# Kernel optimization log

Hardware: AMD Instinct MI355X
Metric: run time of the kernel (lower is better)

Reference implementation:

```python
import jax, jax.numpy as jnp
import numpy as np

N, E = 100000, 1600000
F_IN, F_HID, F_OUT = 64, 64, 16


def setup_inputs() -> dict:
    key = jax.random.key(0)
    ks = jax.random.split(key, 10)
    def g(k, shape):
        return jax.random.normal(k, shape, dtype=jnp.float32) * 0.05
    return {
        "x": jax.random.normal(ks[0], (N, F_IN), dtype=jnp.float32),
        "adj": jax.random.randint(ks[1], (2, E), 0, N, dtype=jnp.int32),
        # ChebConv K=2 params: per-order weights [in, out] + shared bias
        "W1_0": g(ks[2], (F_IN, F_HID)), "W1_1": g(ks[3], (F_IN, F_HID)),
        "b1": jnp.zeros((F_HID,), jnp.float32),
        "Wx_0": g(ks[4], (F_HID, F_HID)), "Wx_1": g(ks[5], (F_HID, F_HID)),
        "bx": jnp.zeros((F_HID,), jnp.float32),
        "W2_0": g(ks[6], (F_HID, F_OUT)), "W2_1": g(ks[7], (F_HID, F_OUT)),
        "b2": jnp.zeros((F_OUT,), jnp.float32),
    }


def _cheb(x, row, col, w, W0, W1, b):
    # K=2 Chebyshev conv: Tx0 = x, Tx1 = L_hat @ x (sparse propagate)
    n = x.shape[0]
    tx1 = jax.ops.segment_sum(w[:, None] * x[col], row, num_segments=n)
    return x @ W0 + tx1 @ W1 + b


def reference(x, adj, W1_0, W1_1, b1, Wx_0, Wx_1, bx, W2_0, W2_1, b2):
    row, col = adj[0], adj[1]
    n = x.shape[0]
    # sym-normalized Laplacian scaled by 2/lambda_max (=1): diagonal cancels,
    # off-diagonal weight = -deg^{-1/2}[row] * deg^{-1/2}[col]
    deg = jax.ops.segment_sum(jnp.ones(adj.shape[1], x.dtype), row, num_segments=n)
    dis = jnp.where(deg > 0, jax.lax.rsqrt(jnp.maximum(deg, 1e-12)), 0.0)
    w = -dis[row] * dis[col]
    h = jax.nn.relu(_cheb(x, row, col, w, W1_0, W1_1, b1))
    # dropout is identity in eval mode
    h = jax.nn.relu(_cheb(h, row, col, w, Wx_0, Wx_1, bx))
    return _cheb(h, row, col, w, W2_0, W2_1, b2)
```

## Files before the change

### kernel.cpp

```cpp
#include <hip/hip_runtime.h>
#include <hip/hip_bf16.h>


#define EPB 4096

typedef __attribute__((ext_vector_type(8))) short bf16x8;
typedef __attribute__((ext_vector_type(4))) float f32x4;

__device__ __forceinline__ float bf2f(unsigned short u) {
    unsigned int x = ((unsigned int)u) << 16;
    return __uint_as_float(x);
}
__device__ __forceinline__ unsigned short f2bf(float f) {
    unsigned int b = __float_as_uint(f);
    unsigned int r = (b + 0x7FFF + ((b >> 16) & 1)) >> 16;
    return (unsigned short)r;
}

__global__ __launch_bounds__(256) void zero_ints(int* __restrict__ p, int n) {
    int i = blockIdx.x * 256 + threadIdx.x;
    if (i < n) p[i] = 0;
}

template <int NC>
__device__ __forceinline__ void pack_pair(const float* __restrict__ W0,
                                          const float* __restrict__ W1,
                                          unsigned short* __restrict__ out, int idx) {
    constexpr int NT = NC / 16;
    int i = idx & 7;
    int m = (idx >> 3) & 15;
    int g = (idx >> 7) & 3;
    int f = idx >> 9;
    int nt = f % NT;
    int kt = f / NT;
    const float* W = (kt < 2) ? W0 : W1;
    int k = (kt & 1) * 32 + g * 8 + i;
    out[idx] = f2bf(W[k * NC + nt * 16 + m]);
}

__global__ __launch_bounds__(256) void wconv_all(const float* __restrict__ W1_0,
                                                 const float* __restrict__ W1_1,
                                                 const float* __restrict__ Wx_0,
                                                 const float* __restrict__ Wx_1,
                                                 const float* __restrict__ W2_0,
                                                 const float* __restrict__ W2_1,
                                                 unsigned short* __restrict__ wp1,
                                                 unsigned short* __restrict__ wpx,
                                                 unsigned short* __restrict__ wp2) {
    int idx = blockIdx.x * 256 + threadIdx.x;
    if (idx < 8192) pack_pair<64>(W1_0, W1_1, wp1, idx);
    else if (idx < 16384) pack_pair<64>(Wx_0, Wx_1, wpx, idx - 8192);
    else if (idx < 18432) pack_pair<16>(W2_0, W2_1, wp2, idx - 16384);
}

__global__ __launch_bounds__(256) void bucket_count(const int* __restrict__ row,
                                                    int* __restrict__ bcnt,
                                                    int e, int nbk) {
    __shared__ int bh[512];
    int tid = threadIdx.x;
    for (int j = tid; j < nbk; j += 256) bh[j] = 0;
    __syncthreads();
    int base = blockIdx.x * EPB;
#pragma unroll
    for (int k = 0; k < EPB / 256; ++k) {
        int i = base + k * 256 + tid;
        if (i < e) atomicAdd(&bh[row[i] >> 8], 1);
    }
    __syncthreads();
    for (int j = tid; j < nbk; j += 256) {
        int c = bh[j];
        if (c) atomicAdd(&bcnt[j], c);
    }
}

__global__ __launch_bounds__(256) void bucket_scan(const int* __restrict__ bcnt,
                                                   int* __restrict__ bbase,
                                                   int* __restrict__ bcursor,
                                                   int* __restrict__ off,
                                                   int nbk, int n, int e) {
    __shared__ int sa[512], sb[512];
    int tid = threadIdx.x;
    for (int j = tid; j < 512; j += 256) sa[j] = (j < nbk) ? bcnt[j] : 0;
    __syncthreads();
    int* in = sa;
    int* out = sb;
    for (int d = 1; d < 512; d <<= 1) {
        for (int j = tid; j < 512; j += 256)
            out[j] = in[j] + ((j >= d) ? in[j - d] : 0);
        __syncthreads();
        int* t = in; in = out; out = t;
    }
    for (int j = tid; j < nbk; j += 256) {
        int incl = in[j];
        int excl = incl - bcnt[j];
        bbase[j] = excl;
        bcursor[j] = excl;
        if (j == nbk - 1) bbase[nbk] = incl;
    }
    if (tid == 0) off[n] = e;
}

__global__ __launch_bounds__(256) void bucket_scatter(const int* __restrict__ row,
                                                      const int* __restrict__ col,
                                                      int* __restrict__ bcursor,
                                                      int* __restrict__ packed,
                                                      int e, int nbk) {
    __shared__ int bh[512];
    __shared__ int bbase[512];
    __shared__ int bcur[512];
    int tid = threadIdx.x;
    for (int j = tid; j < nbk; j += 256) { bh[j] = 0; bcur[j] = 0; }
    __syncthreads();
    int base = blockIdx.x * EPB;
#pragma unroll
    for (int k = 0; k < EPB / 256; ++k) {
        int i = base + k * 256 + tid;
        if (i < e) atomicAdd(&bh[row[i] >> 8], 1);
    }
    __syncthreads();
    for (int j = tid; j < nbk; j += 256) {
        int c = bh[j];
        bbase[j] = c ? atomicAdd(&bcursor[j], c) : 0;
    }
    __syncthreads();
#pragma unroll
    for (int k = 0; k < EPB / 256; ++k) {
        int i = base + k * 256 + tid;
        if (i < e) {
            int r = row[i];
            int b = r >> 8;
            int slot = bbase[b] + atomicAdd(&bcur[b], 1);
            packed[slot] = ((r & 255) << 17) | col[i];
        }
    }
}

__global__ __launch_bounds__(256) void bucket_build(const int* __restrict__ packed,
                                                    const int* __restrict__ bbase,
                                                    const float* __restrict__ x,
                                                    int* __restrict__ off,
                                                    float* __restrict__ dis,
                                                    int* __restrict__ csr,
                                                    unsigned short* __restrict__ y,
                                                    unsigned short* __restrict__ xb,
                                                    int n) {
    __shared__ int rcnt[256];
    __shared__ int sa[256], sb[256];
    __shared__ float disv[256];
    int tid = threadIdx.x;
    int b = blockIdx.x;
    int ebase = bbase[b], eend = bbase[b + 1];
    rcnt[tid] = 0;
    __syncthreads();
    for (int e = ebase + tid; e < eend; e += 256)
        atomicAdd(&rcnt[packed[e] >> 17], 1);
    __syncthreads();
    sa[tid] = rcnt[tid];
    __syncthreads();
    int* in = sa;
    int* out = sb;
    for (int d = 1; d < 256; d <<= 1) {
        out[tid] = in[tid] + ((tid >= d) ? in[tid - d] : 0);
        __syncthreads();
        int* t = in; in = out; out = t;
    }
    int grow = b * 256 + tid;
    int c = rcnt[tid];
    int excl = in[tid] - c;
    float dv = (c > 0) ? rsqrtf((float)c) : 0.0f;
    disv[tid] = dv;
    if (grow < n) {
        off[grow] = ebase + excl;
        dis[grow] = dv;
    }
    out[tid] = excl;
    __syncthreads();
    for (int e = ebase + tid; e < eend; e += 256) {
        int p = packed[e];
        int lr = p >> 17;
        int pos = atomicAdd(&out[lr], 1);
        csr[ebase + pos] = p & 0x1FFFF;
    }
    for (int idx = tid; idx < 4096; idx += 256) {
        int rr = idx >> 4, q = idx & 15;
        int R = b * 256 + rr;
        if (R < n) {
            float d = disv[rr];
            float4 v = ((const float4*)x)[(size_t)R * 16 + q];
            ushort4 o = {f2bf(v.x * d), f2bf(v.y * d), f2bf(v.z * d), f2bf(v.w * d)};
            ((ushort4*)y)[(size_t)R * 16 + q] = o;
            ushort4 xo = {f2bf(v.x), f2bf(v.y), f2bf(v.z), f2bf(v.w)};
            ((ushort4*)xb)[(size_t)R * 16 + q] = xo;
        }
    }
}


__global__ __launch_bounds__(256) void aggregate(const unsigned short* __restrict__ y,
                                                 const int* __restrict__ csr,
                                                 const int* __restrict__ off,
                                                 const float* __restrict__ dis,
                                                 unsigned short* __restrict__ tx, int n) {
    int tid = threadIdx.x;
    int r = blockIdx.x * 16 + (tid >> 4);
    if (r >= n) return;
    int q = tid & 15;
    int s0 = off[r], e1 = off[r + 1];
    const ushort4* Y = (const ushort4*)y;
    float ax = 0.f, ay = 0.f, az = 0.f, aw = 0.f;
    int t = s0;
    for (; t + 8 <= e1; t += 8) {
        int c0 = csr[t], c1 = csr[t + 1], c2 = csr[t + 2], c3 = csr[t + 3];
        int c4 = csr[t + 4], c5 = csr[t + 5], c6 = csr[t + 6], c7 = csr[t + 7];
        ushort4 v0 = Y[(size_t)c0 * 16 + q];
        ushort4 v1 = Y[(size_t)c1 * 16 + q];
        ushort4 v2 = Y[(size_t)c2 * 16 + q];
        ushort4 v3 = Y[(size_t)c3 * 16 + q];
        ushort4 v4 = Y[(size_t)c4 * 16 + q];
        ushort4 v5 = Y[(size_t)c5 * 16 + q];
        ushort4 v6 = Y[(size_t)c6 * 16 + q];
        ushort4 v7 = Y[(size_t)c7 * 16 + q];
        ax += ((bf2f(v0.x) + bf2f(v1.x)) + (bf2f(v2.x) + bf2f(v3.x))) +
              ((bf2f(v4.x) + bf2f(v5.x)) + (bf2f(v6.x) + bf2f(v7.x)));
        ay += ((bf2f(v0.y) + bf2f(v1.y)) + (bf2f(v2.y) + bf2f(v3.y))) +
              ((bf2f(v4.y) + bf2f(v5.y)) + (bf2f(v6.y) + bf2f(v7.y)));
        az += ((bf2f(v0.z) + bf2f(v1.z)) + (bf2f(v2.z) + bf2f(v3.z))) +
              ((bf2f(v4.z) + bf2f(v5.z)) + (bf2f(v6.z) + bf2f(v7.z)));
        aw += ((bf2f(v0.w) + bf2f(v1.w)) + (bf2f(v2.w) + bf2f(v3.w))) +
              ((bf2f(v4.w) + bf2f(v5.w)) + (bf2f(v6.w) + bf2f(v7.w)));
    }
    for (; t + 4 <= e1; t += 4) {
        int c0 = csr[t], c1 = csr[t + 1], c2 = csr[t + 2], c3 = csr[t + 3];
        ushort4 v0 = Y[(size_t)c0 * 16 + q];
        ushort4 v1 = Y[(size_t)c1 * 16 + q];
        ushort4 v2 = Y[(size_t)c2 * 16 + q];
        ushort4 v3 = Y[(size_t)c3 * 16 + q];
        ax += (bf2f(v0.x) + bf2f(v1.x)) + (bf2f(v2.x) + bf2f(v3.x));
        ay += (bf2f(v0.y) + bf2f(v1.y)) + (bf2f(v2.y) + bf2f(v3.y));
        az += (bf2f(v0.z) + bf2f(v1.z)) + (bf2f(v2.z) + bf2f(v3.z));
        aw += (bf2f(v0.w) + bf2f(v1.w)) + (bf2f(v2.w) + bf2f(v3.w));
    }
    for (; t < e1; ++t) {
        int c = csr[t];
        ushort4 v = Y[(size_t)c * 16 + q];
        ax += bf2f(v.x); ay += bf2f(v.y); az += bf2f(v.z); aw += bf2f(v.w);
    }
    float d = -dis[r];
    ushort4 o = {f2bf(ax * d), f2bf(ay * d), f2bf(az * d), f2bf(aw * d)};
    *(ushort4*)&tx[(size_t)r * 64 + q * 4] = o;
}


template <int NC, bool RELU, bool WRITE_HY>
__global__ __launch_bounds__(256) void dense_mfma(const unsigned short* __restrict__ A0,
                                                  const unsigned short* __restrict__ A1,
                                                  const unsigned short* __restrict__ Wp,
                                                  const float* __restrict__ bias,
                                                  const float* __restrict__ dis,
                                                  unsigned short* __restrict__ hout,
                                                  unsigned short* __restrict__ yout,
                                                  float* __restrict__ fout,
                                                  int n, int nrb) {
    constexpr int NT = NC / 16;
    int lane = threadIdx.x & 63;
    int m = lane & 15;
    int g = lane >> 4;
    const bf16x8* WP = (const bf16x8*)Wp;
    bf16x8 bf[NT][4];
#pragma unroll
    for (int kt = 0; kt < 4; ++kt)
#pragma unroll
        for (int nt = 0; nt < NT; ++nt)
            bf[nt][kt] = WP[((kt * NT + nt) * 4 + g) * 16 + m];
    int wrb = blockIdx.x * 4 + (threadIdx.x >> 6);
    int stride = gridDim.x * 4;
    for (int rb = wrb; rb < nrb; rb += stride) {
        int r0 = rb * 16;
        int ra = r0 + m;
        if (ra > n - 1) ra = n - 1;
        const unsigned short* q0 = A0 + (size_t)ra * 64 + g * 8;
        const unsigned short* q1 = A1 + (size_t)ra * 64 + g * 8;
        bf16x8 a0 = *(const bf16x8*)q0;
        bf16x8 a1 = *(const bf16x8*)(q0 + 32);
        bf16x8 a2 = *(const bf16x8*)q1;
        bf16x8 a3 = *(const bf16x8*)(q1 + 32);
        f32x4 acc[NT];
#pragma unroll
        for (int nt = 0; nt < NT; ++nt) {
            float b = bias[nt * 16 + m];
            acc[nt][0] = b; acc[nt][1] = b; acc[nt][2] = b; acc[nt][3] = b;
        }
#pragma unroll
        for (int nt = 0; nt < NT; ++nt) {
            acc[nt] = __builtin_amdgcn_mfma_f32_16x16x32_bf16(a0, bf[nt][0], acc[nt], 0, 0, 0);
            acc[nt] = __builtin_amdgcn_mfma_f32_16x16x32_bf16(a1, bf[nt][1], acc[nt], 0, 0, 0);
            acc[nt] = __builtin_amdgcn_mfma_f32_16x16x32_bf16(a2, bf[nt][2], acc[nt], 0, 0, 0);
            acc[nt] = __builtin_amdgcn_mfma_f32_16x16x32_bf16(a3, bf[nt][3], acc[nt], 0, 0, 0);
        }
#pragma unroll
        for (int reg = 0; reg < 4; ++reg) {
            int rr = r0 + 4 * g + reg;
            if (rr >= n) continue;
            if (WRITE_HY) {
                float dv = dis[rr];
#pragma unroll
                for (int nt = 0; nt < NT; ++nt) {
                    float v = acc[nt][reg];
                    if (RELU) v = fmaxf(v, 0.f);
                    hout[(size_t)rr * NC + nt * 16 + m] = f2bf(v);
                    yout[(size_t)rr * NC + nt * 16 + m] = f2bf(v * dv);
                }
            } else {
#pragma unroll
                for (int nt = 0; nt < NT; ++nt)
                    fout[(size_t)rr * NC + nt * 16 + m] = acc[nt][reg];
            }
        }
    }
}


extern "C" void kernel_launch(void* const* d_in, const int* in_sizes, int n_in,
                              void* d_out, int out_size, void* d_ws, size_t ws_size,
                              hipStream_t stream) {
    const float* x    = (const float*)d_in[0];
    const int*   adj  = (const int*)d_in[1];
    const float* W1_0 = (const float*)d_in[2];
    const float* W1_1 = (const float*)d_in[3];
    const float* b1   = (const float*)d_in[4];
    const float* Wx_0 = (const float*)d_in[5];
    const float* Wx_1 = (const float*)d_in[6];
    const float* bx   = (const float*)d_in[7];
    const float* W2_0 = (const float*)d_in[8];
    const float* W2_1 = (const float*)d_in[9];
    const float* b2   = (const float*)d_in[10];
    float* out = (float*)d_out;

    int N = in_sizes[0] / 64;
    int E = in_sizes[1] / 2;
    const int* row = adj;
    const int* col = adj + E;
    int NBK = (N + 255) / 256;
    int nRB = (N + 15) / 16;

    char* p = (char*)d_ws;
    auto alloc = [&](size_t bytes) {
        char* q = p;
        p += (bytes + 255) & ~(size_t)255;
        return q;
    };
    int*   bcnt  = (int*)alloc((size_t)(NBK) * 4);
    int*   bbase = (int*)alloc((size_t)(NBK + 1) * 4);
    int*   bcur  = (int*)alloc((size_t)(NBK) * 4);
    int*   off   = (int*)alloc((size_t)(N + 1) * 4);
    float* dis   = (float*)alloc((size_t)N * 4);
    int*   csr   = (int*)alloc((size_t)E * 4);
    unsigned short* wp1 = (unsigned short*)alloc(8192 * 2);
    unsigned short* wpx = (unsigned short*)alloc(8192 * 2);
    unsigned short* wp2 = (unsigned short*)alloc(2048 * 2);
    unsigned short* y  = (unsigned short*)alloc((size_t)N * 64 * 2);
    unsigned short* xb = (unsigned short*)alloc((size_t)N * 64 * 2);
    unsigned short* tx = (unsigned short*)alloc((size_t)N * 64 * 2);
    unsigned short* h  = (unsigned short*)alloc((size_t)N * 64 * 2);
    (void)ws_size;
    int* packed = (int*)tx;

    int EB = (E + EPB - 1) / EPB;
    zero_ints<<<(NBK + 255) / 256, 256, 0, stream>>>(bcnt, NBK);
    wconv_all<<<72, 256, 0, stream>>>(W1_0, W1_1, Wx_0, Wx_1, W2_0, W2_1, wp1, wpx, wp2);
    bucket_count<<<EB, 256, 0, stream>>>(row, bcnt, E, NBK);
    bucket_scan<<<1, 256, 0, stream>>>(bcnt, bbase, bcur, off, NBK, N, E);
    bucket_scatter<<<EB, 256, 0, stream>>>(row, col, bcur, packed, E, NBK);
    bucket_build<<<NBK, 256, 0, stream>>>(packed, bbase, x, off, dis, csr, y, xb, N);

    const int DG = 512;
    aggregate<<<(N + 15) / 16, 256, 0, stream>>>(y, csr, off, dis, tx, N);
    dense_mfma<64, true, true><<<DG, 256, 0, stream>>>(xb, tx, wp1, b1, dis, h, y, nullptr, N, nRB);
    aggregate<<<(N + 15) / 16, 256, 0, stream>>>(y, csr, off, dis, tx, N);
    dense_mfma<64, true, true><<<DG, 256, 0, stream>>>(h, tx, wpx, bx, dis, h, y, nullptr, N, nRB);
    aggregate<<<(N + 15) / 16, 256, 0, stream>>>(y, csr, off, dis, tx, N);
    dense_mfma<16, false, false><<<DG, 256, 0, stream>>>(h, tx, wp2, b2, dis, nullptr, nullptr, out, N, nRB);
}
```

Baseline: 202.7 us.

## Fuse sparse aggregation with dense MFMA per layer via LDS tile

Merges each layer's aggregate and dense_mfma kernels into one agg_dense kernel. The aggregated Tx1 tile is kept in swizzled shared memory instead of going through a global tx buffer. The gather now uses 4 threads per row with 16-byte bf16x8 loads, which needs double-buffered y/h arrays to avoid read-after-write hazards between layers. The zero_ints launch is folded into wconv_all. This removes three kernel launches and the tx write/read round trip, at the cost of less parallelism per row in the gather (4 lanes per row instead of 16) and extra workspace.

```diff
diff --git a/kernel.cpp b/kernel.cpp
--- a/kernel.cpp
+++ b/kernel.cpp
@@ -16,10 +16,9 @@
     unsigned int r = (b + 0x7FFF + ((b >> 16) & 1)) >> 16;
     return (unsigned short)r;
 }
-
-__global__ __launch_bounds__(256) void zero_ints(int* __restrict__ p, int n) {
-    int i = blockIdx.x * 256 + threadIdx.x;
-    if (i < n) p[i] = 0;
+__device__ __forceinline__ void acc8(float* a, bf16x8 v) {
+#pragma unroll
+    for (int i = 0; i < 8; ++i) a[i] += bf2f((unsigned short)(short)v[i]);
 }
 
 template <int NC>
@@ -46,8 +45,10 @@
                                                  const float* __restrict__ W2_1,
                                                  unsigned short* __restrict__ wp1,
                                                  unsigned short* __restrict__ wpx,
-                                                 unsigned short* __restrict__ wp2) {
+                                                 unsigned short* __restrict__ wp2,
+                                                 int* __restrict__ bcnt, int nbk) {
     int idx = blockIdx.x * 256 + threadIdx.x;
+    if (idx < nbk) bcnt[idx] = 0;
     if (idx < 8192) pack_pair<64>(W1_0, W1_1, wp1, idx);
     else if (idx < 16384) pack_pair<64>(Wx_0, Wx_1, wpx, idx - 8192);
     else if (idx < 18432) pack_pair<16>(W2_0, W2_1, wp2, idx - 16384);
@@ -196,75 +197,72 @@
 }
 
 
-__global__ __launch_bounds__(256) void aggregate(const unsigned short* __restrict__ y,
+template <int NC, bool RELU, bool WRITE_HY>
+__global__ __launch_bounds__(256) void agg_dense(const unsigned short* __restrict__ y,
+                                                 const unsigned short* __restrict__ A0,
                                                  const int* __restrict__ csr,
                                                  const int* __restrict__ off,
                                                  const float* __restrict__ dis,
-                                                 unsigned short* __restrict__ tx, int n) {
-    int tid = threadIdx.x;
-    int r = blockIdx.x * 16 + (tid >> 4);
-    if (r >= n) return;
-    int q = tid & 15;
-    int s0 = off[r], e1 = off[r + 1];
-    const ushort4* Y = (const ushort4*)y;
-    float ax = 0.f, ay = 0.f, az = 0.f, aw = 0.f;
-    int t = s0;
-    for (; t + 8 <= e1; t += 8) {
-        int c0 = csr[t], c1 = csr[t + 1], c2 = csr[t + 2], c3 = csr[t + 3];
-        int c4 = csr[t + 4], c5 = csr[t + 5], c6 = csr[t + 6], c7 = csr[t + 7];
-        ushort4 v0 = Y[(size_t)c0 * 16 + q];
-        ushort4 v1 = Y[(size_t)c1 * 16 + q];
-        ushort4 v2 = Y[(size_t)c2 * 16 + q];
-        ushort4 v3 = Y[(size_t)c3 * 16 + q];
-        ushort4 v4 = Y[(size_t)c4 * 16 + q];
-        ushort4 v5 = Y[(size_t)c5 * 16 + q];
-        ushort4 v6 = Y[(size_t)c6 * 16 + q];
-        ushort4 v7 = Y[(size_t)c7 * 16 + q];
-        ax += ((bf2f(v0.x) + bf2f(v1.x)) + (bf2f(v2.x) + bf2f(v3.x))) +
-              ((bf2f(v4.x) + bf2f(v5.x)) + (bf2f(v6.x) + bf2f(v7.x)));
-        ay += ((bf2f(v0.y) + bf2f(v1.y)) + (bf2f(v2.y) + bf2f(v3.y))) +
-              ((bf2f(v4.y) + bf2f(v5.y)) + (bf2f(v6.y) + bf2f(v7.y)));
-        az += ((bf2f(v0.z) + bf2f(v1.z)) + (bf2f(v2.z) + bf2f(v3.z))) +
-              ((bf2f(v4.z) + bf2f(v5.z)) + (bf2f(v6.z) + bf2f(v7.z)));
-        aw += ((bf2f(v0.w) + bf2f(v1.w)) + (bf2f(v2.w) + bf2f(v3.w))) +
-              ((bf2f(v4.w) + bf2f(v5.w)) + (bf2f(v6.w) + bf2f(v7.w)));
-    }
-    for (; t + 4 <= e1; t += 4) {
-        int c0 = csr[t], c1 = csr[t + 1], c2 = csr[t + 2], c3 = csr[t + 3];
-        ushort4 v0 = Y[(size_t)c0 * 16 + q];
-        ushort4 v1 = Y[(size_t)c1 * 16 + q];
-        ushort4 v2 = Y[(size_t)c2 * 16 + q];
-        ushort4 v3 = Y[(size_t)c3 * 16 + q];
-        ax += (bf2f(v0.x) + bf2f(v1.x)) + (bf2f(v2.x) + bf2f(v3.x));
-        ay += (bf2f(v0.y) + bf2f(v1.y)) + (bf2f(v2.y) + bf2f(v3.y));
-        az += (bf2f(v0.z) + bf2f(v1.z)) + (bf2f(v2.z) + bf2f(v3.z));
-        aw += (bf2f(v0.w) + bf2f(v1.w)) + (bf2f(v2.w) + bf2f(v3.w));
-    }
-    for (; t < e1; ++t) {
-        int c = csr[t];
-        ushort4 v = Y[(size_t)c * 16 + q];
-        ax += bf2f(v.x); ay += bf2f(v.y); az += bf2f(v.z); aw += bf2f(v.w);
-    }
-    float d = -dis[r];
-    ushort4 o = {f2bf(ax * d), f2bf(ay * d), f2bf(az * d), f2bf(aw * d)};
-    *(ushort4*)&tx[(size_t)r * 64 + q * 4] = o;
-}
-
-
-template <int NC, bool RELU, bool WRITE_HY>
-__global__ __launch_bounds__(256) void dense_mfma(const unsigned short* __restrict__ A0,
-                                                  const unsigned short* __restrict__ A1,
-                                                  const unsigned short* __restrict__ Wp,
-                                                  const float* __restrict__ bias,
-                                                  const float* __restrict__ dis,
-                                                  unsigned short* __restrict__ hout,
-                                                  unsigned short* __restrict__ yout,
-                                                  float* __restrict__ fout,
-                                                  int n, int nrb) {
+                                                 const unsigned short* __restrict__ Wp,
+                                                 const float* __restrict__ bias,
+                                                 unsigned short* __restrict__ hout,
+                                                 unsigned short* __restrict__ yout,
+                                                 float* __restrict__ fout,
+                                                 int n) {
     constexpr int NT = NC / 16;
-    int lane = threadIdx.x & 63;
+    __shared__ unsigned short txl[64 * 64];
+    int tid = threadIdx.x;
+
+    int row_l = tid >> 2;
+    int fq = tid & 3;
+    int r = blockIdx.x * 64 + row_l;
+    float acc16[16];
+#pragma unroll
+    for (int i = 0; i < 16; ++i) acc16[i] = 0.f;
+    float d = 0.f;
+    if (r < n) {
+        int s0 = off[r], e1 = off[r + 1];
+        const unsigned short* Yb = y + fq * 16;
+        int t = s0;
+        for (; t + 4 <= e1; t += 4) {
+            int c0 = csr[t], c1 = csr[t + 1], c2 = csr[t + 2], c3 = csr[t + 3];
+            const bf16x8* p0 = (const bf16x8*)(Yb + (size_t)c0 * 64);
+            const bf16x8* p1 = (const bf16x8*)(Yb + (size_t)c1 * 64);
+            const bf16x8* p2 = (const bf16x8*)(Yb + (size_t)c2 * 64);
+            const bf16x8* p3 = (const bf16x8*)(Yb + (size_t)c3 * 64);
+            bf16x8 v00 = p0[0], v01 = p0[1];
+            bf16x8 v10 = p1[0], v11 = p1[1];
+            bf16x8 v20 = p2[0], v21 = p2[1];
+            bf16x8 v30 = p3[0], v31 = p3[1];
+            acc8(acc16, v00); acc8(acc16 + 8, v01);
+            acc8(acc16, v10); acc8(acc16 + 8, v11);
+            acc8(acc16, v20); acc8(acc16 + 8, v21);
+            acc8(acc16, v30); acc8(acc16 + 8, v31);
+        }
+        for (; t < e1; ++t) {
+            int c = csr[t];
+            const bf16x8* pc = (const bf16x8*)(Yb + (size_t)c * 64);
+            bf16x8 v0 = pc[0], v1 = pc[1];
+            acc8(acc16, v0); acc8(acc16 + 8, v1);
+        }
+        d = -dis[r];
+    }
+    bf16x8 ov0, ov1;
+#pragma unroll
+    for (int i = 0; i < 8; ++i) {
+        ov0[i] = (short)f2bf(acc16[i] * d);
+        ov1[i] = (short)f2bf(acc16[8 + i] * d);
+    }
+    int swz = (row_l & 7) << 4;
+    int cb = fq * 32;
+    *(bf16x8*)((char*)txl + row_l * 128 + (cb ^ swz)) = ov0;
+    *(bf16x8*)((char*)txl + row_l * 128 + ((cb + 16) ^ swz)) = ov1;
+    __syncthreads();
+
+    int lane = tid & 63;
     int m = lane & 15;
     int g = lane >> 4;
+    int w = tid >> 6;
     const bf16x8* WP = (const bf16x8*)Wp;
     bf16x8 bf[NT][4];
 #pragma unroll
@@ -272,49 +270,46 @@
 #pragma unroll
         for (int nt = 0; nt < NT; ++nt)
             bf[nt][kt] = WP[((kt * NT + nt) * 4 + g) * 16 + m];
-    int wrb = blockIdx.x * 4 + (threadIdx.x >> 6);
-    int stride = gridDim.x * 4;
-    for (int rb = wrb; rb < nrb; rb += stride) {
-        int r0 = rb * 16;
-        int ra = r0 + m;
-        if (ra > n - 1) ra = n - 1;
-        const unsigned short* q0 = A0 + (size_t)ra * 64 + g * 8;
-        const unsigned short* q1 = A1 + (size_t)ra * 64 + g * 8;
-        bf16x8 a0 = *(const bf16x8*)q0;
-        bf16x8 a1 = *(const bf16x8*)(q0 + 32);
-        bf16x8 a2 = *(const bf16x8*)q1;
-        bf16x8 a3 = *(const bf16x8*)(q1 + 32);
-        f32x4 acc[NT];
-#pragma unroll
-        for (int nt = 0; nt < NT; ++nt) {
-            float b = bias[nt * 16 + m];
-            acc[nt][0] = b; acc[nt][1] = b; acc[nt][2] = b; acc[nt][3] = b;
-        }
-#pragma unroll
-        for (int nt = 0; nt < NT; ++nt) {
-            acc[nt] = __builtin_amdgcn_mfma_f32_16x16x32_bf16(a0, bf[nt][0], acc[nt], 0, 0, 0);
-            acc[nt] = __builtin_amdgcn_mfma_f32_16x16x32_bf16(a1, bf[nt][1], acc[nt], 0, 0, 0);
-            acc[nt] = __builtin_amdgcn_mfma_f32_16x16x32_bf16(a2, bf[nt][2], acc[nt], 0, 0, 0);
-            acc[nt] = __builtin_amdgcn_mfma_f32_16x16x32_bf16(a3, bf[nt][3], acc[nt], 0, 0, 0);
-        }
-#pragma unroll
-        for (int reg = 0; reg < 4; ++reg) {
-            int rr = r0 + 4 * g + reg;
-            if (rr >= n) continue;
-            if (WRITE_HY) {
-                float dv = dis[rr];
-#pragma unroll
-                for (int nt = 0; nt < NT; ++nt) {
-                    float v = acc[nt][reg];
-                    if (RELU) v = fmaxf(v, 0.f);
-                    hout[(size_t)rr * NC + nt * 16 + m] = f2bf(v);
-                    yout[(size_t)rr * NC + nt * 16 + m] = f2bf(v * dv);
-                }
-            } else {
-#pragma unroll
-                for (int nt = 0; nt < NT; ++nt)
-                    fout[(size_t)rr * NC + nt * 16 + m] = acc[nt][reg];
+    int r0 = blockIdx.x * 64 + w * 16;
+    int ra = r0 + m;
+    if (ra > n - 1) ra = n - 1;
+    const unsigned short* q0 = A0 + (size_t)ra * 64 + g * 8;
+    bf16x8 a0 = *(const bf16x8*)q0;
+    bf16x8 a1 = *(const bf16x8*)(q0 + 32);
+    int rl2 = w * 16 + m;
+    int sw2 = (m & 7) << 4;
+    bf16x8 a2 = *(bf16x8*)((char*)txl + rl2 * 128 + ((g * 16) ^ sw2));
+    bf16x8 a3 = *(bf16x8*)((char*)txl + rl2 * 128 + ((64 + g * 16) ^ sw2));
+    f32x4 acc[NT];
+#pragma unroll
+    for (int nt = 0; nt < NT; ++nt) {
+        float b = bias[nt * 16 + m];
+        acc[nt][0] = b; acc[nt][1] = b; acc[nt][2] = b; acc[nt][3] = b;
+    }
+#pragma unroll
+    for (int nt = 0; nt < NT; ++nt) {
+        acc[nt] = __builtin_amdgcn_mfma_f32_16x16x32_bf16(a0, bf[nt][0], acc[nt], 0, 0, 0);
+        acc[nt] = __builtin_amdgcn_mfma_f32_16x16x32_bf16(a1, bf[nt][1], acc[nt], 0, 0, 0);
+        acc[nt] = __builtin_amdgcn_mfma_f32_16x16x32_bf16(a2, bf[nt][2], acc[nt], 0, 0, 0);
+        acc[nt] = __builtin_amdgcn_mfma_f32_16x16x32_bf16(a3, bf[nt][3], acc[nt], 0, 0, 0);
+    }
+#pragma unroll
+    for (int reg = 0; reg < 4; ++reg) {
+        int rr = r0 + 4 * g + reg;
+        if (rr >= n) continue;
+        if (WRITE_HY) {
+            float dv = dis[rr];
+#pragma unroll
+            for (int nt = 0; nt < NT; ++nt) {
+                float v = acc[nt][reg];
+                if (RELU) v = fmaxf(v, 0.f);
+                hout[(size_t)rr * NC + nt * 16 + m] = f2bf(v);
+                yout[(size_t)rr * NC + nt * 16 + m] = f2bf(v * dv);
             }
+        } else {
+#pragma unroll
+            for (int nt = 0; nt < NT; ++nt)
+                fout[(size_t)rr * NC + nt * 16 + m] = acc[nt][reg];
         }
     }
 }
@@ -341,7 +336,6 @@
     const int* row = adj;
     const int* col = adj + E;
     int NBK = (N + 255) / 256;
-    int nRB = (N + 15) / 16;
 
     char* p = (char*)d_ws;
     auto alloc = [&](size_t bytes) {
@@ -355,29 +349,27 @@
     int*   off   = (int*)alloc((size_t)(N + 1) * 4);
     float* dis   = (float*)alloc((size_t)N * 4);
     int*   csr   = (int*)alloc((size_t)E * 4);
+    int*   packed = (int*)alloc((size_t)E * 4);
     unsigned short* wp1 = (unsigned short*)alloc(8192 * 2);
     unsigned short* wpx = (unsigned short*)alloc(8192 * 2);
     unsigned short* wp2 = (unsigned short*)alloc(2048 * 2);
     unsigned short* y  = (unsigned short*)alloc((size_t)N * 64 * 2);
+    unsigned short* y2 = (unsigned short*)alloc((size_t)N * 64 * 2);
     unsigned short* xb = (unsigned short*)alloc((size_t)N * 64 * 2);
-    unsigned short* tx = (unsigned short*)alloc((size_t)N * 64 * 2);
     unsigned short* h  = (unsigned short*)alloc((size_t)N * 64 * 2);
+    unsigned short* h2 = (unsigned short*)alloc((size_t)N * 64 * 2);
     (void)ws_size;
-    int* packed = (int*)tx;
 
     int EB = (E + EPB - 1) / EPB;
-    zero_ints<<<(NBK + 255) / 256, 256, 0, stream>>>(bcnt, NBK);
-    wconv_all<<<72, 256, 0, stream>>>(W1_0, W1_1, Wx_0, Wx_1, W2_0, W2_1, wp1, wpx, wp2);
+    wconv_all<<<72, 256, 0, stream>>>(W1_0, W1_1, Wx_0, Wx_1, W2_0, W2_1,
+                                      wp1, wpx, wp2, bcnt, NBK);
     bucket_count<<<EB, 256, 0, stream>>>(row, bcnt, E, NBK);
     bucket_scan<<<1, 256, 0, stream>>>(bcnt, bbase, bcur, off, NBK, N, E);
     bucket_scatter<<<EB, 256, 0, stream>>>(row, col, bcur, packed, E, NBK);
     bucket_build<<<NBK, 256, 0, stream>>>(packed, bbase, x, off, dis, csr, y, xb, N);
 
-    const int DG = 512;
-    aggregate<<<(N + 15) / 16, 256, 0, stream>>>(y, csr, off, dis, tx, N);
-    dense_mfma<64, true, true><<<DG, 256, 0, stream>>>(xb, tx, wp1, b1, dis, h, y, nullptr, N, nRB);
-    aggregate<<<(N + 15) / 16, 256, 0, stream>>>(y, csr, off, dis, tx, N);
-    dense_mfma<64, true, true><<<DG, 256, 0, stream>>>(h, tx, wpx, bx, dis, h, y, nullptr, N, nRB);
-    aggregate<<<(N + 15) / 16, 256, 0, stream>>>(y, csr, off, dis, tx, N);
-    dense_mfma<16, false, false><<<DG, 256, 0, stream>>>(h, tx, wp2, b2, dis, nullptr, nullptr, out, N, nRB);
-}
+    int nb64 = (N + 63) / 64;
+    agg_dense<64, true, true><<<nb64, 256, 0, stream>>>(y, xb, csr, off, dis, wp1, b1, h, y2, nullptr, N);
+    agg_dense<64, true, true><<<nb64, 256, 0, stream>>>(y2, h, csr, off, dis, wpx, bx, h2, y, nullptr, N);
+    agg_dense<16, false, false><<<nb64, 256, 0, stream>>>(y, h2, csr, off, dis, wp2, b2, nullptr, nullptr, out, N);
+}
```

Result: faster. 188.3 us (-7.1%).
